# Optimization experiments

Measured on AMD Instinct MI355X. Metric: run time of the kernel, lower is better.

## Reference

```python
import jax, jax.numpy as jnp
import numpy as np

FFT_SIZE = 1024
HOP = 256

def _dft_weights(fft_size):
    # Matches torch module: np.fft.fft(np.eye(N)) * np.hanning(N)
    # fft_mat[k, n] = exp(-2j*pi*k*n/N) * hanning[n]
    fft_mat = np.fft.fft(np.eye(fft_size)) * np.hanning(fft_size)
    real_w = jnp.asarray(np.real(fft_mat), dtype=jnp.float32)  # [N, N]
    imag_w = jnp.asarray(np.imag(fft_mat), dtype=jnp.float32)  # [N, N]
    return real_w, imag_w

def setup_inputs() -> dict:
    key = jax.random.key(0)
    x = jax.random.normal(key, (32, 160000), dtype=jnp.float32)
    real_w, imag_w = _dft_weights(FFT_SIZE)
    return {"x": x, "real_w": real_w, "imag_w": imag_w}

def reference(x, real_w, imag_w):
    N = FFT_SIZE
    hop = HOP
    B, L = x.shape
    n_frames = (L - N) // hop + 1
    # Frame extraction: frames[b, t, n] = x[b, t*hop + n]
    idx = jnp.arange(n_frames)[:, None] * hop + jnp.arange(N)[None, :]  # [T, N]
    frames = x[:, idx]  # [B, T, N]
    # DFT-as-GEMM (same math as Conv1d(1, N, N, stride=hop) with DFT weights)
    real_x = jnp.einsum('btn,kn->bkt', frames, real_w)  # [B, N, T]
    imag_x = jnp.einsum('btn,kn->bkt', frames, imag_w)  # [B, N, T]
    mag = (real_x ** 2 + imag_x ** 2)[:, :N // 2 + 1, :]  # [B, N//2+1, T]
    phase = jnp.arctan2(imag_x, real_x)  # [B, N, T]
    return (mag, phase)
```

## Files before the change

kernel.cpp:

```cpp
#include <hip/hip_runtime.h>
#include <math.h>

#define NFFT     1024
#define HOP      256
#define NFRAMES  622
#define NBATCH   32
#define XLEN     160000
#define TILE_T   8
#define NPAIR    4
#define ROW      1234
#define KBINS    513
#define NT       256
#define NTILES   78
#define NBLK     (NTILES*NBATCH)

#define ZIDX(j,i) ((j)*ROW + (i) + 2*((i)>>4) + 4*((i)>>6) + 8*((i)>>8))

#define C1 0.9238795325112867f
#define S1 0.3826834323650898f
#define C2 0.7071067811865476f
#define STEP (-0.006135923151542565f)

__device__ __forceinline__ float2 cmul(float2 a, float2 b) {
    return make_float2(a.x*b.x - a.y*b.y, a.x*b.y + a.y*b.x);
}
__device__ __forceinline__ float2 csqr(float2 a) {
    return make_float2(a.x*a.x - a.y*a.y, 2.0f*a.x*a.y);
}

__device__ __forceinline__ void bfly4(float2& a, float2& b, float2& c, float2& d,
                                      float2 w1, float2 w2, float2 w3) {
    float2 apc = make_float2(a.x + c.x, a.y + c.y);
    float2 amc = make_float2(a.x - c.x, a.y - c.y);
    float2 bpd = make_float2(b.x + d.x, b.y + d.y);
    float2 bmd = make_float2(b.x - d.x, b.y - d.y);
    float2 y0 = make_float2(apc.x + bpd.x, apc.y + bpd.y);
    float2 y2 = make_float2(apc.x - bpd.x, apc.y - bpd.y);
    float2 y1 = make_float2(amc.x + bmd.y, amc.y - bmd.x);
    float2 y3 = make_float2(amc.x - bmd.y, amc.y + bmd.x);
    a = y0; b = cmul(w1, y1); c = cmul(w2, y2); d = cmul(w3, y3);
}
__device__ __forceinline__ void bfly4_nw(float2& a, float2& b, float2& c, float2& d) {
    float2 apc = make_float2(a.x + c.x, a.y + c.y);
    float2 amc = make_float2(a.x - c.x, a.y - c.y);
    float2 bpd = make_float2(b.x + d.x, b.y + d.y);
    float2 bmd = make_float2(b.x - d.x, b.y - d.y);
    a = make_float2(apc.x + bpd.x, apc.y + bpd.y);
    b = make_float2(amc.x + bmd.y, amc.y - bmd.x);
    c = make_float2(apc.x - bpd.x, apc.y - bpd.y);
    d = make_float2(amc.x - bmd.y, amc.y + bmd.x);
}

__device__ __forceinline__ int rev4(int k) {
    return ((k & 3) << 8) | ((k & 12) << 4) | (k & 48) | ((k >> 4) & 12) | ((k >> 8) & 3);
}

__device__ __forceinline__ void fence() {
    asm volatile("s_waitcnt lgkmcnt(0)" ::: "memory");
    __builtin_amdgcn_sched_barrier(0);
}

__device__ __forceinline__ float fast_atan2f(float y, float x) {
    const float ax = fabsf(x), ay = fabsf(y);
    const float mx = fmaxf(ax, ay), mn = fminf(ax, ay);
    float r = mn / mx;
    if (mx == 0.0f) r = 0.0f;
    const float t = r * r;
    float p = fmaf(t, -0.01172120f, 0.05265332f);
    p = fmaf(t, p, -0.11643287f);
    p = fmaf(t, p, 0.19354346f);
    p = fmaf(t, p, -0.33262347f);
    p = fmaf(t, p, 0.99997726f);
    float a = r * p;
    a = (ay > ax) ? (1.5707963267948966f - a) : a;
    a = (x < 0.0f) ? (3.14159265358979323f - a) : a;
    return copysignf(a, y);
}

__global__ __launch_bounds__(NT, 4)
void spec_kernel(const float* __restrict__ x, const float* __restrict__ win,
                 float* __restrict__ out)
{
    __shared__ __align__(16) float2 zb[NPAIR * ROW];

    const int tid = threadIdx.x;
    const int lg  = (blockIdx.x & 7) * (NBLK / 8) + (blockIdx.x >> 3);
    const int b   = lg / NTILES;
    const int t0  = (lg - b * NTILES) * TILE_T;
    const int wv  = tid >> 6;
    const int ln  = tid & 63;

    {
        const int f0 = t0 + 2*wv, f1 = f0 + 1;
        const float* xb = x + (size_t)b * XLEN;
        const bool v0 = (f0 < NFRAMES), v1 = (f1 < NFRAMES);
        #pragma unroll
        for (int q = 0; q < 4; ++q) {
            const int n0 = (q << 8) + (ln << 2);
            const float4 w4 = *reinterpret_cast<const float4*>(&win[n0]);
            float4 a4 = make_float4(0.f, 0.f, 0.f, 0.f), b4 = a4;
            if (v0) a4 = *reinterpret_cast<const float4*>(&xb[f0*HOP + n0]);
            if (v1) b4 = *reinterpret_cast<const float4*>(&xb[f1*HOP + n0]);
            float4* dst = reinterpret_cast<float4*>(&zb[ZIDX(wv, n0)]);
            dst[0] = make_float4(w4.x*a4.x, w4.x*b4.x, w4.y*a4.y, w4.y*b4.y);
            dst[1] = make_float4(w4.z*a4.z, w4.z*b4.z, w4.w*a4.w, w4.w*b4.w);
        }
    }
    fence();

    {
        float2 E[16];
        #pragma unroll
        for (int j = 0; j < 16; ++j) E[j] = zb[ZIDX(wv, (j << 6) + ln)];
        float sw, cw;
        sincosf(STEP * (float)ln, &sw, &cw);
        const float2 wc = make_float2(cw, sw);
        #pragma unroll
        for (int q = 0; q < 4; ++q) {
            float2 w1;
            if      (q == 0) w1 = wc;
            else if (q == 1) w1 = cmul(wc, make_float2(C1, -S1));
            else if (q == 2) w1 = cmul(wc, make_float2(C2, -C2));
            else             w1 = cmul(wc, make_float2(S1, -C1));
            float2 w2 = csqr(w1), w3 = cmul(w1, w2);
            bfly4(E[q], E[q+4], E[q+8], E[q+12], w1, w2, w3);
        }
        const float2 wb  = csqr(csqr(wc));
        const float2 wb2 = csqr(wb), wb3 = cmul(wb, wb2);
        #pragma unroll
        for (int u = 0; u < 4; ++u)
            bfly4(E[4*u], E[4*u+1], E[4*u+2], E[4*u+3], wb, wb2, wb3);
        #pragma unroll
        for (int j = 0; j < 16; ++j) zb[ZIDX(wv, (j << 6) + ln)] = E[j];
    }
    fence();

    {
        const int m = ln & 15, h = ln >> 4;
        float sm, cm;
        sincosf((STEP * 16.0f) * (float)m, &sm, &cm);
        const float2 w1 = make_float2(cm, sm);
        const float2 w2 = csqr(w1), w3 = cmul(w1, w2);
        #pragma unroll
        for (int u = 0; u < 4; ++u) {
            const int base = 256*u + 64*h + m;
            float2 a  = zb[ZIDX(wv, base)],      bb = zb[ZIDX(wv, base + 16)];
            float2 cc = zb[ZIDX(wv, base + 32)], dd = zb[ZIDX(wv, base + 48)];
            bfly4(a, bb, cc, dd, w1, w2, w3);
            zb[ZIDX(wv, base)]      = a;  zb[ZIDX(wv, base + 16)] = bb;
            zb[ZIDX(wv, base + 32)] = cc; zb[ZIDX(wv, base + 48)] = dd;
        }
    }
    fence();

    {
        float2 F[16];
        const float4* src = reinterpret_cast<const float4*>(&zb[ZIDX(wv, ln << 4)]);
        #pragma unroll
        for (int r = 0; r < 8; ++r) {
            const float4 v = src[r];
            F[2*r]   = make_float2(v.x, v.y);
            F[2*r+1] = make_float2(v.z, v.w);
        }
        bfly4_nw(F[0], F[4], F[8],  F[12]);
        bfly4(F[1], F[5], F[9],  F[13], make_float2(C1,-S1), make_float2(C2,-C2), make_float2(S1,-C1));
        bfly4(F[2], F[6], F[10], F[14], make_float2(C2,-C2), make_float2(0.f,-1.f), make_float2(-C2,-C2));
        bfly4(F[3], F[7], F[11], F[15], make_float2(S1,-C1), make_float2(-C2,-C2), make_float2(-C1, S1));
        bfly4_nw(F[0],  F[1],  F[2],  F[3]);
        bfly4_nw(F[4],  F[5],  F[6],  F[7]);
        bfly4_nw(F[8],  F[9],  F[10], F[11]);
        bfly4_nw(F[12], F[13], F[14], F[15]);
        float4* dst = reinterpret_cast<float4*>(&zb[ZIDX(wv, ln << 4)]);
        #pragma unroll
        for (int r = 0; r < 8; ++r)
            dst[r] = make_float4(F[2*r].x, F[2*r].y, F[2*r+1].x, F[2*r+1].y);
    }
    __syncthreads();

    const int kg  = tid >> 2;
    const int jj  = tid & 3;
    const int t_e = t0 + 2*jj;
    const bool tval = (t_e < NFRAMES);

    const int R1 = rev4(kg);
    const int km = 64 - kg;
    const int R2 = ((km & 3) << 8) | ((km & 12) << 4) | (km & 48);
    const int J0 = (kg == 0) ? 16 : 15;
    const float2* zp1 = &zb[ZIDX(jj, R1)];
    const float2* zp2 = &zb[ZIDX(jj, R2)];

    float* magp = out;
    float* php  = out + (size_t)NBATCH * KBINS * NFRAMES;
    const size_t magbase = (size_t)b * KBINS * NFRAMES + t_e;
    const size_t phbase  = (size_t)b * NFFT  * NFRAMES + t_e;

    #pragma unroll
    for (int it = 0; it < 9; ++it) {
        if (it == 8 && kg != 0) break;
        const int k  = kg + (it << 6);
        const int c1 = ((it & 3) << 2) | (it >> 2);
        const int j2 = (J0 - it) & 15;
        const int c2 = ((j2 & 3) << 2) | (j2 >> 2);
        const float2 z1 = zp1[c1];
        const float2 z2 = zp2[c2];
        const float re_e = 0.5f*(z1.x + z2.x);
        const float im_e = 0.5f*(z1.y - z2.y);
        const float re_o = 0.5f*(z1.y + z2.y);
        const float im_o = 0.5f*(z2.x - z1.x);
        if (tval) {
            *reinterpret_cast<float2*>(&magp[magbase + (size_t)k * NFRAMES]) =
                make_float2(fmaf(re_e, re_e, im_e*im_e), fmaf(re_o, re_o, im_o*im_o));
            const float ph_e = fast_atan2f(im_e, re_e);
            const float ph_o = fast_atan2f(im_o, re_o);
            *reinterpret_cast<float2*>(&php[phbase + (size_t)k * NFRAMES]) =
                make_float2(ph_e, ph_o);
            if (k != 0 && k != 512) {
                *reinterpret_cast<float2*>(&php[phbase + (size_t)(NFFT - k) * NFRAMES]) =
                    make_float2(-ph_e, -ph_o);
            }
        }
    }
}

extern "C" void kernel_launch(void* const* d_in, const int* in_sizes, int n_in,
                              void* d_out, int out_size, void* d_ws, size_t ws_size,
                              hipStream_t stream) {
    const float* x  = (const float*)d_in[0];
    const float* rw = (const float*)d_in[1];
    float* out = (float*)d_out;
    spec_kernel<<<dim3(NBLK, 1, 1), dim3(NT, 1, 1), 0, stream>>>(x, rw, out);
}
```

Baseline: 43.19 us.

## Double frames per block, use hardware sin/cos and rcp, precompute LDS offsets

Doubles the frame tile to 16 frames per block (512 threads, 8 frame pairs), halving the number of blocks and making each output row segment longer for the store phase. It replaces sincosf with raw v_sin/v_cos instructions that take revolutions, and the atan2 division with a hardware reciprocal. It also precomputes the padded LDS pointers per stage so the index arithmetic is simpler. The tval guard is hoisted around the whole output loop. Costs are more LDS per block with fewer resident blocks, and slightly lower precision in twiddles and atan2.

```diff
diff --git a/kernel.cpp b/kernel.cpp
--- a/kernel.cpp
+++ b/kernel.cpp
@@ -6,26 +6,32 @@
 #define NFRAMES  622
 #define NBATCH   32
 #define XLEN     160000
-#define TILE_T   8
-#define NPAIR    4
+#define TILE_T   16
+#define NPAIR    8
 #define ROW      1234
 #define KBINS    513
-#define NT       256
-#define NTILES   78
+#define NT       512
+#define NTILES   39
 #define NBLK     (NTILES*NBATCH)
 
-#define ZIDX(j,i) ((j)*ROW + (i) + 2*((i)>>4) + 4*((i)>>6) + 8*((i)>>8))
+#define PAD(i)   ((i) + 2*((i)>>4) + 4*((i)>>6) + 8*((i)>>8))
 
 #define C1 0.9238795325112867f
 #define S1 0.3826834323650898f
 #define C2 0.7071067811865476f
-#define STEP (-0.006135923151542565f)
 
 __device__ __forceinline__ float2 cmul(float2 a, float2 b) {
     return make_float2(a.x*b.x - a.y*b.y, a.x*b.y + a.y*b.x);
 }
 __device__ __forceinline__ float2 csqr(float2 a) {
     return make_float2(a.x*a.x - a.y*a.y, 2.0f*a.x*a.y);
+}
+
+__device__ __forceinline__ float2 w_of_rev(float f) {
+    float s, c;
+    asm("v_sin_f32 %0, %1" : "=v"(s) : "v"(f));
+    asm("v_cos_f32 %0, %1" : "=v"(c) : "v"(f));
+    return make_float2(c, s);
 }
 
 __device__ __forceinline__ void bfly4(float2& a, float2& b, float2& c, float2& d,
@@ -51,10 +57,6 @@
     d = make_float2(amc.x - bmd.y, amc.y + bmd.x);
 }
 
-__device__ __forceinline__ int rev4(int k) {
-    return ((k & 3) << 8) | ((k & 12) << 4) | (k & 48) | ((k >> 4) & 12) | ((k >> 8) & 3);
-}
-
 __device__ __forceinline__ void fence() {
     asm volatile("s_waitcnt lgkmcnt(0)" ::: "memory");
     __builtin_amdgcn_sched_barrier(0);
@@ -63,7 +65,7 @@
 __device__ __forceinline__ float fast_atan2f(float y, float x) {
     const float ax = fabsf(x), ay = fabsf(y);
     const float mx = fmaxf(ax, ay), mn = fminf(ax, ay);
-    float r = mn / mx;
+    float r = mn * __builtin_amdgcn_rcpf(mx);
     if (mx == 0.0f) r = 0.0f;
     const float t = r * r;
     float p = fmaf(t, -0.01172120f, 0.05265332f);
@@ -94,6 +96,8 @@
         const int f0 = t0 + 2*wv, f1 = f0 + 1;
         const float* xb = x + (size_t)b * XLEN;
         const bool v0 = (f0 < NFRAMES), v1 = (f1 < NFRAMES);
+        float4* D4 = reinterpret_cast<float4*>(
+            &zb[wv*ROW + 4*ln + 2*(ln>>2) + 4*(ln>>4)]);
         #pragma unroll
         for (int q = 0; q < 4; ++q) {
             const int n0 = (q << 8) + (ln << 2);
@@ -101,20 +105,18 @@
             float4 a4 = make_float4(0.f, 0.f, 0.f, 0.f), b4 = a4;
             if (v0) a4 = *reinterpret_cast<const float4*>(&xb[f0*HOP + n0]);
             if (v1) b4 = *reinterpret_cast<const float4*>(&xb[f1*HOP + n0]);
-            float4* dst = reinterpret_cast<float4*>(&zb[ZIDX(wv, n0)]);
-            dst[0] = make_float4(w4.x*a4.x, w4.x*b4.x, w4.y*a4.y, w4.y*b4.y);
-            dst[1] = make_float4(w4.z*a4.z, w4.z*b4.z, w4.w*a4.w, w4.w*b4.w);
+            D4[156*q]     = make_float4(w4.x*a4.x, w4.x*b4.x, w4.y*a4.y, w4.y*b4.y);
+            D4[156*q + 1] = make_float4(w4.z*a4.z, w4.z*b4.z, w4.w*a4.w, w4.w*b4.w);
         }
     }
     fence();
 
     {
+        float2* p = &zb[wv*ROW + ln + 2*(ln>>4)];
         float2 E[16];
         #pragma unroll
-        for (int j = 0; j < 16; ++j) E[j] = zb[ZIDX(wv, (j << 6) + ln)];
-        float sw, cw;
-        sincosf(STEP * (float)ln, &sw, &cw);
-        const float2 wc = make_float2(cw, sw);
+        for (int j = 0; j < 16; ++j) E[j] = p[76*j + 8*(j>>2)];
+        const float2 wc = w_of_rev((float)ln * (-1.0f/1024.0f));
         #pragma unroll
         for (int q = 0; q < 4; ++q) {
             float2 w1;
@@ -125,40 +127,39 @@
             float2 w2 = csqr(w1), w3 = cmul(w1, w2);
             bfly4(E[q], E[q+4], E[q+8], E[q+12], w1, w2, w3);
         }
-        const float2 wb  = csqr(csqr(wc));
+        const float2 wb  = w_of_rev((float)ln * (-4.0f/1024.0f));
         const float2 wb2 = csqr(wb), wb3 = cmul(wb, wb2);
         #pragma unroll
         for (int u = 0; u < 4; ++u)
             bfly4(E[4*u], E[4*u+1], E[4*u+2], E[4*u+3], wb, wb2, wb3);
         #pragma unroll
-        for (int j = 0; j < 16; ++j) zb[ZIDX(wv, (j << 6) + ln)] = E[j];
+        for (int j = 0; j < 16; ++j) p[76*j + 8*(j>>2)] = E[j];
     }
     fence();
 
     {
         const int m = ln & 15, h = ln >> 4;
-        float sm, cm;
-        sincosf((STEP * 16.0f) * (float)m, &sm, &cm);
-        const float2 w1 = make_float2(cm, sm);
+        float2* p = &zb[wv*ROW + 76*h + m];
+        const float2 w1 = w_of_rev((float)m * (-1.0f/64.0f));
         const float2 w2 = csqr(w1), w3 = cmul(w1, w2);
         #pragma unroll
         for (int u = 0; u < 4; ++u) {
-            const int base = 256*u + 64*h + m;
-            float2 a  = zb[ZIDX(wv, base)],      bb = zb[ZIDX(wv, base + 16)];
-            float2 cc = zb[ZIDX(wv, base + 32)], dd = zb[ZIDX(wv, base + 48)];
+            float2 a  = p[312*u],      bb = p[312*u + 18];
+            float2 cc = p[312*u + 36], dd = p[312*u + 54];
             bfly4(a, bb, cc, dd, w1, w2, w3);
-            zb[ZIDX(wv, base)]      = a;  zb[ZIDX(wv, base + 16)] = bb;
-            zb[ZIDX(wv, base + 32)] = cc; zb[ZIDX(wv, base + 48)] = dd;
+            p[312*u]      = a;  p[312*u + 18] = bb;
+            p[312*u + 36] = cc; p[312*u + 54] = dd;
         }
     }
     fence();
 
     {
+        float4* p = reinterpret_cast<float4*>(
+            &zb[wv*ROW + 18*ln + 4*(ln>>2) + 8*(ln>>4)]);
         float2 F[16];
-        const float4* src = reinterpret_cast<const float4*>(&zb[ZIDX(wv, ln << 4)]);
         #pragma unroll
         for (int r = 0; r < 8; ++r) {
-            const float4 v = src[r];
+            const float4 v = p[r];
             F[2*r]   = make_float2(v.x, v.y);
             F[2*r+1] = make_float2(v.z, v.w);
         }
@@ -170,44 +171,43 @@
         bfly4_nw(F[4],  F[5],  F[6],  F[7]);
         bfly4_nw(F[8],  F[9],  F[10], F[11]);
         bfly4_nw(F[12], F[13], F[14], F[15]);
-        float4* dst = reinterpret_cast<float4*>(&zb[ZIDX(wv, ln << 4)]);
         #pragma unroll
         for (int r = 0; r < 8; ++r)
-            dst[r] = make_float4(F[2*r].x, F[2*r].y, F[2*r+1].x, F[2*r+1].y);
+            p[r] = make_float4(F[2*r].x, F[2*r].y, F[2*r+1].x, F[2*r+1].y);
     }
     __syncthreads();
 
-    const int kg  = tid >> 2;
-    const int jj  = tid & 3;
+    const int kg  = tid >> 3;
+    const int jj  = tid & 7;
     const int t_e = t0 + 2*jj;
     const bool tval = (t_e < NFRAMES);
 
-    const int R1 = rev4(kg);
+    const int R1 = ((kg & 3) << 8) | ((kg & 12) << 4) | (kg & 48);
     const int km = 64 - kg;
     const int R2 = ((km & 3) << 8) | ((km & 12) << 4) | (km & 48);
     const int J0 = (kg == 0) ? 16 : 15;
-    const float2* zp1 = &zb[ZIDX(jj, R1)];
-    const float2* zp2 = &zb[ZIDX(jj, R2)];
+    const float2* zp1 = &zb[jj*ROW + PAD(R1)];
+    const float2* zp2 = &zb[jj*ROW + PAD(R2)];
 
     float* magp = out;
     float* php  = out + (size_t)NBATCH * KBINS * NFRAMES;
     const size_t magbase = (size_t)b * KBINS * NFRAMES + t_e;
     const size_t phbase  = (size_t)b * NFFT  * NFRAMES + t_e;
 
-    #pragma unroll
-    for (int it = 0; it < 9; ++it) {
-        if (it == 8 && kg != 0) break;
-        const int k  = kg + (it << 6);
-        const int c1 = ((it & 3) << 2) | (it >> 2);
-        const int j2 = (J0 - it) & 15;
-        const int c2 = ((j2 & 3) << 2) | (j2 >> 2);
-        const float2 z1 = zp1[c1];
-        const float2 z2 = zp2[c2];
-        const float re_e = 0.5f*(z1.x + z2.x);
-        const float im_e = 0.5f*(z1.y - z2.y);
-        const float re_o = 0.5f*(z1.y + z2.y);
-        const float im_o = 0.5f*(z2.x - z1.x);
-        if (tval) {
+    if (tval) {
+        #pragma unroll
+        for (int it = 0; it < 9; ++it) {
+            if (it == 8 && kg != 0) break;
+            const int k  = kg + (it << 6);
+            const int c1 = ((it & 3) << 2) | (it >> 2);
+            const int j2 = (J0 - it) & 15;
+            const int c2 = ((j2 & 3) << 2) | (j2 >> 2);
+            const float2 z1 = zp1[c1];
+            const float2 z2 = zp2[c2];
+            const float re_e = 0.5f*(z1.x + z2.x);
+            const float im_e = 0.5f*(z1.y - z2.y);
+            const float re_o = 0.5f*(z1.y + z2.y);
+            const float im_o = 0.5f*(z2.x - z1.x);
             *reinterpret_cast<float2*>(&magp[magbase + (size_t)k * NFRAMES]) =
                 make_float2(fmaf(re_e, re_e, im_e*im_e), fmaf(re_o, re_o, im_o*im_o));
             const float ph_e = fast_atan2f(im_e, re_e);
```

Result: faster. 40.27 us (-6.8%).
